# Kernel optimization log

Hardware: AMD Instinct MI355X
Metric: run time of the kernel (lower is better)

Reference implementation:

```python
import jax, jax.numpy as jnp
import numpy as np

W = 4           # cp_size (simulated ranks)
NUM_HEADS = 32
HEAD_SIZE = 128
NUM_KV_HEADS = 8
BLOCK_SIZE = 16
NUM_BLOCKS = 1024
MAX_BLOCKS = 32
MAX_CTX = 512   # <= _PARTITION_SIZE so single-partition stats are exact
NUM_SEQS = 32
SCALE = 1.0 / np.sqrt(HEAD_SIZE)
NEG_INF = -1e30


def setup_inputs() -> dict:
    key = jax.random.key(0)
    k1, k2, k3, k4, k5 = jax.random.split(key, 5)
    query = jax.random.normal(k1, (NUM_SEQS, 1, NUM_HEADS * HEAD_SIZE), dtype=jnp.float32)
    # per-rank paged KV caches, layout [W, num_blocks, kv_heads, block_size, head_size]
    key_cache = jax.random.normal(k2, (W, NUM_BLOCKS, NUM_KV_HEADS, BLOCK_SIZE, HEAD_SIZE), dtype=jnp.float32)
    value_cache = jax.random.normal(k3, (W, NUM_BLOCKS, NUM_KV_HEADS, BLOCK_SIZE, HEAD_SIZE), dtype=jnp.float32)
    block_tables = jax.random.randint(k4, (W, NUM_SEQS, MAX_BLOCKS), 0, NUM_BLOCKS, dtype=jnp.int32)
    context_lens = jax.random.randint(k5, (W, NUM_SEQS), 1, MAX_CTX + 1, dtype=jnp.int32)
    return {"query": query, "key_cache": key_cache, "value_cache": value_cache,
            "block_tables": block_tables, "context_lens": context_lens}


def reference(query, key_cache, value_cache, block_tables, context_lens):
    B, L, _ = query.shape
    S = B * L                       # num_seqs (decode: L=1)
    G = NUM_KV_HEADS
    Q = NUM_HEADS // G              # queries per kv head
    T = MAX_BLOCKS * BLOCK_SIZE     # max context per rank

    q = query.reshape(S, G, Q, HEAD_SIZE)
    ridx = jnp.arange(W)[:, None, None]
    # gather paged blocks: [W, S, MAX_BLOCKS, G, BLOCK_SIZE, D] -> [W, S, G, T, D]
    k = key_cache[ridx, block_tables].transpose(0, 1, 3, 2, 4, 5).reshape(W, S, G, T, HEAD_SIZE)
    v = value_cache[ridx, block_tables].transpose(0, 1, 3, 2, 4, 5).reshape(W, S, G, T, HEAD_SIZE)

    logits = jnp.einsum('sgqd,wsgtd->wsgqt', q, k) * SCALE
    mask = jnp.arange(T)[None, None, None, None, :] < context_lens[:, :, None, None, None]
    logits = jnp.where(mask, logits, NEG_INF)

    # per-rank online-softmax stats (== paged_attention_v2 single-partition output)
    m = jnp.max(logits, axis=-1)                      # [W,S,G,Q] max logit per rank
    p = jnp.exp(logits - m[..., None])
    p = jnp.where(mask, p, 0.0)
    esum = jnp.sum(p, axis=-1)                        # [W,S,G,Q]
    out_r = jnp.einsum('wsgqt,wsgtd->wsgqd', p, v) / esum[..., None]  # normalized per-rank out

    # cross-rank log-sum-exp reduction (distributed_paged_attention_v2_reduce)
    gmax = jnp.max(m, axis=0)                         # [S,G,Q]
    w_r = esum * jnp.exp(m - gmax[None])              # [W,S,G,Q]
    out = jnp.sum(out_r * w_r[..., None], axis=0) / jnp.sum(w_r, axis=0)[..., None]

    return out.reshape(B, L, NUM_HEADS * HEAD_SIZE)
```

## Files before the change

### kernel.cpp

```cpp
#include <hip/hip_runtime.h>
#include <math.h>

#define W 4
#define NUM_HEADS 32
#define HEAD_SIZE 128
#define G 8
#define QPG 4
#define BLOCK_SZ 16
#define NUM_BLOCKS 1024
#define MAX_BLOCKS 32
#define S 32
#define SPLIT 2
#define NPART (W * SPLIT)
#define SCALE 0.08838834764831845f
#define NEG_BIG (-1e30f)
#define L2E 1.4426950408889634f
#define K1L2E (SCALE * L2E)
#define RESCALE_MARGIN 4.0f

#define BLK_STRIDE (G * BLOCK_SZ * HEAD_SIZE)
#define WG_STRIDE  (NUM_BLOCKS * BLK_STRIDE)

template <int CTRL>
__device__ __forceinline__ float dpp_fold(float x) {
    const int y = __builtin_amdgcn_update_dpp(0, __float_as_int(x), CTRL, 0xF, 0xF, true);
    return x + __int_as_float(y);
}

__device__ __forceinline__ float half_allsum(float x) {
    x = dpp_fold<0xB1>(x);
    x = dpp_fold<0x4E>(x);
    x = dpp_fold<0x141>(x);
    x = dpp_fold<0x140>(x);
    x += __shfl_xor(x, 16);
    return x;
}

__global__ __launch_bounds__(256, 5)
void pa_partial_kernel(const float* __restrict__ query,
                       const float* __restrict__ key_cache,
                       const float* __restrict__ value_cache,
                       const int* __restrict__ block_tables,
                       const int* __restrict__ context_lens,
                       float* __restrict__ acc_ws,
                       float* __restrict__ m_ws,
                       float* __restrict__ e_ws)
{
    int bx = blockIdx.x;
    const int p = bx % SPLIT; bx /= SPLIT;
    const int g = bx % G;     bx /= G;
    const int s = bx % S;
    const int w = bx / S;

    const int tid   = threadIdx.x;
    const int accid = tid >> 5;
    const int lane  = tid & 31;
    const int d0    = lane * 4;
    const int h     = accid + 8 * p;

    __shared__ int   bt_lds[MAX_BLOCKS];
    __shared__ float sm_m[8];
    __shared__ float sm_e[8][QPG];
    __shared__ float sm_acc[8][QPG][HEAD_SIZE];

    if (tid < MAX_BLOCKS)
        bt_lds[tid] = block_tables[((size_t)w * S + s) * MAX_BLOCKS + tid];
    __syncthreads();

    float4 qf[QPG];
#pragma unroll
    for (int qi = 0; qi < QPG; ++qi)
        qf[qi] = *reinterpret_cast<const float4*>(
            query + ((size_t)s * NUM_HEADS + g * QPG + qi) * HEAD_SIZE + d0);

    const int ctx = context_lens[w * S + s];
    const float* kbase = key_cache   + (size_t)w * WG_STRIDE + (size_t)g * BLOCK_SZ * HEAD_SIZE;
    const float* vbase = value_cache + (size_t)w * WG_STRIDE + (size_t)g * BLOCK_SZ * HEAD_SIZE;

    float m_run = NEG_BIG;
    float bexp  = 0.f;
    float e_i[QPG];
    float4 acc[QPG];
#pragma unroll
    for (int qi = 0; qi < QPG; ++qi) {
        e_i[qi] = 0.f;
        acc[qi] = make_float4(0.f, 0.f, 0.f, 0.f);
    }

    int t = h;
    for (; t + 16 < ctx; t += 32) {
        const int slot = (t & 15) * HEAD_SIZE + d0;
        const int off1 = bt_lds[t >> 4] * BLK_STRIDE + slot;
        const int off2 = bt_lds[(t >> 4) + 1] * BLK_STRIDE + slot;
        const float4 k1 = *reinterpret_cast<const float4*>(kbase + off1);
        const float4 k2 = *reinterpret_cast<const float4*>(kbase + off2);
        const float4 v1 = *reinterpret_cast<const float4*>(vbase + off1);
        const float4 v2 = *reinterpret_cast<const float4*>(vbase + off2);

        float dA[QPG], dB[QPG];
#pragma unroll
        for (int qi = 0; qi < QPG; ++qi) {
            dA[qi] = qf[qi].x*k1.x + qf[qi].y*k1.y + qf[qi].z*k1.z + qf[qi].w*k1.w;
            dB[qi] = qf[qi].x*k2.x + qf[qi].y*k2.y + qf[qi].z*k2.z + qf[qi].w*k2.w;
        }
#pragma unroll
        for (int qi = 0; qi < QPG; ++qi) {
            dA[qi] = half_allsum(dA[qi]);
            dB[qi] = half_allsum(dB[qi]);
        }

        float mraw = fmaxf(fmaxf(dA[0], dA[1]), fmaxf(dA[2], dA[3]));
        mraw = fmaxf(mraw, fmaxf(fmaxf(dB[0], dB[1]), fmaxf(dB[2], dB[3])));
        const float mx = mraw * SCALE;
        if (mx > m_run) {
            const float newm  = mx + RESCALE_MARGIN;
            const float alpha = exp2f((m_run - newm) * L2E);
            m_run = newm;
            bexp  = -m_run * L2E;
#pragma unroll
            for (int qi = 0; qi < QPG; ++qi) {
                e_i[qi] *= alpha;
                acc[qi].x *= alpha; acc[qi].y *= alpha;
                acc[qi].z *= alpha; acc[qi].w *= alpha;
            }
        }
#pragma unroll
        for (int qi = 0; qi < QPG; ++qi) {
            const float p1 = exp2f(fmaf(dA[qi], K1L2E, bexp));
            const float p2 = exp2f(fmaf(dB[qi], K1L2E, bexp));
            e_i[qi] += p1 + p2;
            acc[qi].x = fmaf(p2, v2.x, fmaf(p1, v1.x, acc[qi].x));
            acc[qi].y = fmaf(p2, v2.y, fmaf(p1, v1.y, acc[qi].y));
            acc[qi].z = fmaf(p2, v2.z, fmaf(p1, v1.z, acc[qi].z));
            acc[qi].w = fmaf(p2, v2.w, fmaf(p1, v1.w, acc[qi].w));
        }
    }
    if (t < ctx) {
        const int off1 = bt_lds[t >> 4] * BLK_STRIDE + (t & 15) * HEAD_SIZE + d0;
        const float4 k1 = *reinterpret_cast<const float4*>(kbase + off1);
        const float4 v1 = *reinterpret_cast<const float4*>(vbase + off1);
        float dA[QPG];
#pragma unroll
        for (int qi = 0; qi < QPG; ++qi)
            dA[qi] = qf[qi].x*k1.x + qf[qi].y*k1.y + qf[qi].z*k1.z + qf[qi].w*k1.w;
#pragma unroll
        for (int qi = 0; qi < QPG; ++qi)
            dA[qi] = half_allsum(dA[qi]);
        const float mx = SCALE * fmaxf(fmaxf(dA[0], dA[1]), fmaxf(dA[2], dA[3]));
        if (mx > m_run) {
            const float newm  = mx + RESCALE_MARGIN;
            const float alpha = exp2f((m_run - newm) * L2E);
            m_run = newm;
            bexp  = -m_run * L2E;
#pragma unroll
            for (int qi = 0; qi < QPG; ++qi) {
                e_i[qi] *= alpha;
                acc[qi].x *= alpha; acc[qi].y *= alpha;
                acc[qi].z *= alpha; acc[qi].w *= alpha;
            }
        }
#pragma unroll
        for (int qi = 0; qi < QPG; ++qi) {
            const float p1 = exp2f(fmaf(dA[qi], K1L2E, bexp));
            e_i[qi] += p1;
            acc[qi].x = fmaf(p1, v1.x, acc[qi].x);
            acc[qi].y = fmaf(p1, v1.y, acc[qi].y);
            acc[qi].z = fmaf(p1, v1.z, acc[qi].z);
            acc[qi].w = fmaf(p1, v1.w, acc[qi].w);
        }
    }

    if (lane == 0) sm_m[accid] = m_run;
#pragma unroll
    for (int qi = 0; qi < QPG; ++qi) {
        if (lane == 0) sm_e[accid][qi] = e_i[qi];
        sm_acc[accid][qi][d0 + 0] = acc[qi].x;
        sm_acc[accid][qi][d0 + 1] = acc[qi].y;
        sm_acc[accid][qi][d0 + 2] = acc[qi].z;
        sm_acc[accid][qi][d0 + 3] = acc[qi].w;
    }
    __syncthreads();

    const int r = w * SPLIT + p;
    float gm = NEG_BIG;
#pragma unroll
    for (int hh = 0; hh < 8; ++hh) gm = fmaxf(gm, sm_m[hh]);
    float sc[8];
#pragma unroll
    for (int hh = 0; hh < 8; ++hh) sc[hh] = __expf(sm_m[hh] - gm);

    for (int pi = tid; pi < QPG * HEAD_SIZE; pi += 256) {
        const int qi = pi >> 7;
        const int d  = pi & (HEAD_SIZE - 1);
        float num = 0.f, den = 0.f;
#pragma unroll
        for (int hh = 0; hh < 8; ++hh) {
            num += sm_acc[hh][qi][d] * sc[hh];
            den += sm_e[hh][qi] * sc[hh];
        }
        const size_t idx = (((size_t)r * S + s) * G + g) * QPG + qi;
        acc_ws[idx * HEAD_SIZE + d] = num;
        if (d == 0) { m_ws[idx] = gm; e_ws[idx] = den; }
    }
}

__global__ __launch_bounds__(256)
void pa_reduce_kernel(const float* __restrict__ acc_ws,
                      const float* __restrict__ m_ws,
                      const float* __restrict__ e_ws,
                      float* __restrict__ out)
{
    const int bx = blockIdx.x;
    const int s = bx / G, g = bx % G;
    const int tid = threadIdx.x;
    for (int pi = tid; pi < QPG * HEAD_SIZE; pi += 256) {
        const int qi = pi >> 7;
        const int d  = pi & (HEAD_SIZE - 1);
        float mw[NPART], ew[NPART];
        float gm = NEG_BIG;
#pragma unroll
        for (int r = 0; r < NPART; ++r) {
            const size_t idx = (((size_t)r * S + s) * G + g) * QPG + qi;
            mw[r] = m_ws[idx];
            ew[r] = e_ws[idx];
            gm = fmaxf(gm, mw[r]);
        }
        float num = 0.f, den = 0.f;
#pragma unroll
        for (int r = 0; r < NPART; ++r) {
            const float sc = __expf(mw[r] - gm);
            const size_t idx = (((size_t)r * S + s) * G + g) * QPG + qi;
            num += acc_ws[idx * HEAD_SIZE + d] * sc;
            den += ew[r] * sc;
        }
        out[((size_t)s * NUM_HEADS + g * QPG + qi) * HEAD_SIZE + d] = num / den;
    }
}

__global__ __launch_bounds__(256)
void pa_fused_kernel(const float* __restrict__ query,
                     const float* __restrict__ key_cache,
                     const float* __restrict__ value_cache,
                     const int* __restrict__ block_tables,
                     const int* __restrict__ context_lens,
                     float* __restrict__ out)
{
    const int bx = blockIdx.x;
    const int s = bx / G, g = bx % G;
    const int tid   = threadIdx.x;
    const int accid = tid >> 5;
    const int lane  = tid & 31;
    const int d0    = lane * 4;

    __shared__ int   bt_lds[MAX_BLOCKS];
    __shared__ float sm_m[8][QPG];
    __shared__ float sm_e[8][QPG];
    __shared__ float sm_acc[8][QPG][HEAD_SIZE];

    float4 qf[QPG];
#pragma unroll
    for (int qi = 0; qi < QPG; ++qi)
        qf[qi] = *reinterpret_cast<const float4*>(
            query + ((size_t)s * NUM_HEADS + g * QPG + qi) * HEAD_SIZE + d0);

    float  m_i[QPG], e_i[QPG];
    float4 acc[QPG];
#pragma unroll
    for (int qi = 0; qi < QPG; ++qi) {
        m_i[qi] = NEG_BIG; e_i[qi] = 0.f;
        acc[qi] = make_float4(0.f, 0.f, 0.f, 0.f);
    }

    for (int w = 0; w < W; ++w) {
        __syncthreads();
        if (tid < MAX_BLOCKS)
            bt_lds[tid] = block_tables[((size_t)w * S + s) * MAX_BLOCKS + tid];
        __syncthreads();
        const int ctx = context_lens[w * S + s];
        const float* kbase = key_cache   + (size_t)w * WG_STRIDE + (size_t)g * BLOCK_SZ * HEAD_SIZE;
        const float* vbase = value_cache + (size_t)w * WG_STRIDE + (size_t)g * BLOCK_SZ * HEAD_SIZE;
        for (int t = accid; t < ctx; t += 8) {
            const int off = bt_lds[t >> 4] * BLK_STRIDE + (t & 15) * HEAD_SIZE + d0;
            const float4 kx = *reinterpret_cast<const float4*>(kbase + off);
            const float4 vx = *reinterpret_cast<const float4*>(vbase + off);
            float dv[QPG];
#pragma unroll
            for (int qi = 0; qi < QPG; ++qi)
                dv[qi] = qf[qi].x*kx.x + qf[qi].y*kx.y + qf[qi].z*kx.z + qf[qi].w*kx.w;
#pragma unroll
            for (int qi = 0; qi < QPG; ++qi)
                dv[qi] = half_allsum(dv[qi]);
#pragma unroll
            for (int qi = 0; qi < QPG; ++qi) {
                const float lg    = dv[qi] * SCALE;
                const float mn    = fmaxf(m_i[qi], lg);
                const float alpha = __expf(m_i[qi] - mn);
                const float pp    = __expf(lg - mn);
                m_i[qi] = mn;
                e_i[qi] = e_i[qi] * alpha + pp;
                acc[qi].x = fmaf(acc[qi].x, alpha, pp * vx.x);
                acc[qi].y = fmaf(acc[qi].y, alpha, pp * vx.y);
                acc[qi].z = fmaf(acc[qi].z, alpha, pp * vx.z);
                acc[qi].w = fmaf(acc[qi].w, alpha, pp * vx.w);
            }
        }
    }

#pragma unroll
    for (int qi = 0; qi < QPG; ++qi) {
        if (lane == 0) { sm_m[accid][qi] = m_i[qi]; sm_e[accid][qi] = e_i[qi]; }
        sm_acc[accid][qi][d0 + 0] = acc[qi].x;
        sm_acc[accid][qi][d0 + 1] = acc[qi].y;
        sm_acc[accid][qi][d0 + 2] = acc[qi].z;
        sm_acc[accid][qi][d0 + 3] = acc[qi].w;
    }
    __syncthreads();

    for (int pi = tid; pi < QPG * HEAD_SIZE; pi += 256) {
        const int qi = pi >> 7;
        const int d  = pi & (HEAD_SIZE - 1);
        float gm = NEG_BIG;
#pragma unroll
        for (int hh = 0; hh < 8; ++hh) gm = fmaxf(gm, sm_m[hh][qi]);
        float num = 0.f, den = 0.f;
#pragma unroll
        for (int hh = 0; hh < 8; ++hh) {
            const float sc = __expf(sm_m[hh][qi] - gm);
            num += sm_acc[hh][qi][d] * sc;
            den += sm_e[hh][qi] * sc;
        }
        out[((size_t)s * NUM_HEADS + g * QPG + qi) * HEAD_SIZE + d] = num / den;
    }
}

extern "C" void kernel_launch(void* const* d_in, const int* in_sizes, int n_in,
                              void* d_out, int out_size, void* d_ws, size_t ws_size,
                              hipStream_t stream) {
    const float* query        = (const float*)d_in[0];
    const float* key_cache    = (const float*)d_in[1];
    const float* value_cache  = (const float*)d_in[2];
    const int*   block_tables = (const int*)d_in[3];
    const int*   context_lens = (const int*)d_in[4];
    float* out = (float*)d_out;

    const size_t n_acc   = (size_t)NPART * S * G * QPG * HEAD_SIZE;
    const size_t n_stats = (size_t)NPART * S * G * QPG;
    const size_t need    = (n_acc + 2 * n_stats) * sizeof(float);

    if (ws_size >= need) {
        float* acc_ws = (float*)d_ws;
        float* m_ws   = acc_ws + n_acc;
        float* e_ws   = m_ws + n_stats;
        pa_partial_kernel<<<W * S * G * SPLIT, 256, 0, stream>>>(
            query, key_cache, value_cache, block_tables, context_lens,
            acc_ws, m_ws, e_ws);
        pa_reduce_kernel<<<S * G, 256, 0, stream>>>(acc_ws, m_ws, e_ws, out);
    } else {
        pa_fused_kernel<<<S * G, 256, 0, stream>>>(
            query, key_cache, value_cache, block_tables, context_lens, out);
    }
}
```

Before: 459.4 us.

## Split context four ways and software-pipeline KV loads in partial attention

Raises the context split per rank from two to four partitions, giving more workgroups, and changes how tokens are assigned to threads in the inner loop. The loop now prefetches the next pair of K/V float4 rows before computing on the current pair, to hide global-memory latency. A final odd token is handled inside the same loop by masking the second logit instead of a separate tail. The cost is more registers (the launch bound is lowered to allow this), lower occupancy, and a larger cross-partition reduction.

Result: no change. 460.0 us (+0.1%).

```diff
diff --git a/kernel.cpp b/kernel.cpp
--- a/kernel.cpp
+++ b/kernel.cpp
@@ -10,8 +10,10 @@
 #define NUM_BLOCKS 1024
 #define MAX_BLOCKS 32
 #define S 32
-#define SPLIT 2
+#define SPLIT 4
 #define NPART (W * SPLIT)
+#define TS (8 * SPLIT)
+#define PAIR (2 * TS)
 #define SCALE 0.08838834764831845f
 #define NEG_BIG (-1e30f)
 #define L2E 1.4426950408889634f
@@ -36,7 +38,7 @@
     return x;
 }
 
-__global__ __launch_bounds__(256, 5)
+__global__ __launch_bounds__(256, 4)
 void pa_partial_kernel(const float* __restrict__ query,
                        const float* __restrict__ key_cache,
                        const float* __restrict__ value_cache,
@@ -88,85 +90,79 @@
     }
 
     int t = h;
-    for (; t + 16 < ctx; t += 32) {
-        const int slot = (t & 15) * HEAD_SIZE + d0;
-        const int off1 = bt_lds[t >> 4] * BLK_STRIDE + slot;
-        const int off2 = bt_lds[(t >> 4) + 1] * BLK_STRIDE + slot;
-        const float4 k1 = *reinterpret_cast<const float4*>(kbase + off1);
-        const float4 k2 = *reinterpret_cast<const float4*>(kbase + off2);
-        const float4 v1 = *reinterpret_cast<const float4*>(vbase + off1);
-        const float4 v2 = *reinterpret_cast<const float4*>(vbase + off2);
-
-        float dA[QPG], dB[QPG];
-#pragma unroll
-        for (int qi = 0; qi < QPG; ++qi) {
-            dA[qi] = qf[qi].x*k1.x + qf[qi].y*k1.y + qf[qi].z*k1.z + qf[qi].w*k1.w;
-            dB[qi] = qf[qi].x*k2.x + qf[qi].y*k2.y + qf[qi].z*k2.z + qf[qi].w*k2.w;
-        }
-#pragma unroll
-        for (int qi = 0; qi < QPG; ++qi) {
-            dA[qi] = half_allsum(dA[qi]);
-            dB[qi] = half_allsum(dB[qi]);
-        }
-
-        float mraw = fmaxf(fmaxf(dA[0], dA[1]), fmaxf(dA[2], dA[3]));
-        mraw = fmaxf(mraw, fmaxf(fmaxf(dB[0], dB[1]), fmaxf(dB[2], dB[3])));
-        const float mx = mraw * SCALE;
-        if (mx > m_run) {
-            const float newm  = mx + RESCALE_MARGIN;
-            const float alpha = exp2f((m_run - newm) * L2E);
-            m_run = newm;
-            bexp  = -m_run * L2E;
-#pragma unroll
-            for (int qi = 0; qi < QPG; ++qi) {
-                e_i[qi] *= alpha;
-                acc[qi].x *= alpha; acc[qi].y *= alpha;
-                acc[qi].z *= alpha; acc[qi].w *= alpha;
+    if (t < ctx) {
+        const int slot = (h & 15) * HEAD_SIZE + d0;
+        bool pair = (t + TS) < ctx;
+        {
+            const int b1 = t >> 4;
+            const int o1 = bt_lds[b1] * BLK_STRIDE + slot;
+            const int o2 = pair ? (bt_lds[b1 + (TS / 16)] * BLK_STRIDE + slot) : o1;
+            float4 k1 = *reinterpret_cast<const float4*>(kbase + o1);
+            float4 v1 = *reinterpret_cast<const float4*>(vbase + o1);
+            float4 k2 = *reinterpret_cast<const float4*>(kbase + o2);
+            float4 v2 = *reinterpret_cast<const float4*>(vbase + o2);
+
+            for (;;) {
+                const int  tn     = t + PAIR;
+                const bool n_any  = tn < ctx;
+                const bool n_pair = (tn + TS) < ctx;
+                float4 nk1, nv1, nk2, nv2;
+                if (n_any) {
+                    const int nb1 = tn >> 4;
+                    const int no1 = bt_lds[nb1] * BLK_STRIDE + slot;
+                    const int no2 = n_pair ? (bt_lds[nb1 + (TS / 16)] * BLK_STRIDE + slot) : no1;
+                    nk1 = *reinterpret_cast<const float4*>(kbase + no1);
+                    nv1 = *reinterpret_cast<const float4*>(vbase + no1);
+                    nk2 = *reinterpret_cast<const float4*>(kbase + no2);
+                    nv2 = *reinterpret_cast<const float4*>(vbase + no2);
+                }
+
+                float dA[QPG], dB[QPG];
+#pragma unroll
+                for (int qi = 0; qi < QPG; ++qi) {
+                    dA[qi] = qf[qi].x*k1.x + qf[qi].y*k1.y + qf[qi].z*k1.z + qf[qi].w*k1.w;
+                    dB[qi] = qf[qi].x*k2.x + qf[qi].y*k2.y + qf[qi].z*k2.z + qf[qi].w*k2.w;
+                }
+#pragma unroll
+                for (int qi = 0; qi < QPG; ++qi) {
+                    dA[qi] = half_allsum(dA[qi]);
+                    dB[qi] = half_allsum(dB[qi]);
+                }
+                if (!pair) {
+#pragma unroll
+                    for (int qi = 0; qi < QPG; ++qi) dB[qi] = NEG_BIG;
+                }
+
+                float mraw = fmaxf(fmaxf(dA[0], dA[1]), fmaxf(dA[2], dA[3]));
+                mraw = fmaxf(mraw, fmaxf(fmaxf(dB[0], dB[1]), fmaxf(dB[2], dB[3])));
+                const float mx = mraw * SCALE;
+                if (mx > m_run) {
+                    const float newm  = mx + RESCALE_MARGIN;
+                    const float alpha = exp2f((m_run - newm) * L2E);
+                    m_run = newm;
+                    bexp  = -m_run * L2E;
+#pragma unroll
+                    for (int qi = 0; qi < QPG; ++qi) {
+                        e_i[qi] *= alpha;
+                        acc[qi].x *= alpha; acc[qi].y *= alpha;
+                        acc[qi].z *= alpha; acc[qi].w *= alpha;
+                    }
+                }
+#pragma unroll
+                for (int qi = 0; qi < QPG; ++qi) {
+                    const float p1 = exp2f(fmaf(dA[qi], K1L2E, bexp));
+                    const float p2 = exp2f(fmaf(dB[qi], K1L2E, bexp));
+                    e_i[qi] += p1 + p2;
+                    acc[qi].x = fmaf(p2, v2.x, fmaf(p1, v1.x, acc[qi].x));
+                    acc[qi].y = fmaf(p2, v2.y, fmaf(p1, v1.y, acc[qi].y));
+                    acc[qi].z = fmaf(p2, v2.z, fmaf(p1, v1.z, acc[qi].z));
+                    acc[qi].w = fmaf(p2, v2.w, fmaf(p1, v1.w, acc[qi].w));
+                }
+
+                if (!n_any) break;
+                t = tn; pair = n_pair;
+                k1 = nk1; v1 = nv1; k2 = nk2; v2 = nv2;
             }
-        }
-#pragma unroll
-        for (int qi = 0; qi < QPG; ++qi) {
-            const float p1 = exp2f(fmaf(dA[qi], K1L2E, bexp));
-            const float p2 = exp2f(fmaf(dB[qi], K1L2E, bexp));
-            e_i[qi] += p1 + p2;
-            acc[qi].x = fmaf(p2, v2.x, fmaf(p1, v1.x, acc[qi].x));
-            acc[qi].y = fmaf(p2, v2.y, fmaf(p1, v1.y, acc[qi].y));
-            acc[qi].z = fmaf(p2, v2.z, fmaf(p1, v1.z, acc[qi].z));
-            acc[qi].w = fmaf(p2, v2.w, fmaf(p1, v1.w, acc[qi].w));
-        }
-    }
-    if (t < ctx) {
-        const int off1 = bt_lds[t >> 4] * BLK_STRIDE + (t & 15) * HEAD_SIZE + d0;
-        const float4 k1 = *reinterpret_cast<const float4*>(kbase + off1);
-        const float4 v1 = *reinterpret_cast<const float4*>(vbase + off1);
-        float dA[QPG];
-#pragma unroll
-        for (int qi = 0; qi < QPG; ++qi)
-            dA[qi] = qf[qi].x*k1.x + qf[qi].y*k1.y + qf[qi].z*k1.z + qf[qi].w*k1.w;
-#pragma unroll
-        for (int qi = 0; qi < QPG; ++qi)
-            dA[qi] = half_allsum(dA[qi]);
-        const float mx = SCALE * fmaxf(fmaxf(dA[0], dA[1]), fmaxf(dA[2], dA[3]));
-        if (mx > m_run) {
-            const float newm  = mx + RESCALE_MARGIN;
-            const float alpha = exp2f((m_run - newm) * L2E);
-            m_run = newm;
-            bexp  = -m_run * L2E;
-#pragma unroll
-            for (int qi = 0; qi < QPG; ++qi) {
-                e_i[qi] *= alpha;
-                acc[qi].x *= alpha; acc[qi].y *= alpha;
-                acc[qi].z *= alpha; acc[qi].w *= alpha;
-            }
-        }
-#pragma unroll
-        for (int qi = 0; qi < QPG; ++qi) {
-            const float p1 = exp2f(fmaf(dA[qi], K1L2E, bexp));
-            e_i[qi] += p1;
-            acc[qi].x = fmaf(p1, v1.x, acc[qi].x);
-            acc[qi].y = fmaf(p1, v1.y, acc[qi].y);
-            acc[qi].z = fmaf(p1, v1.z, acc[qi].z);
-            acc[qi].w = fmaf(p1, v1.w, acc[qi].w);
         }
     }
 
```
